# Optimization experiments

Measured on AMD Instinct MI355X. Metric: run time of the kernel, lower is better.

Reference implementation:

```python
import jax, jax.numpy as jnp
import numpy as np

B, F, HU, HC = 8192, 100, 128, 512


def _lin(key, din, dout, bias=True, scale=0.02):
    k1, k2 = jax.random.split(key)
    w = jax.random.normal(k1, (din, dout), jnp.float32) * scale
    if bias:
        b = jax.random.normal(k2, (dout,), jnp.float32) * scale
        return w, b
    return (w,)


def setup_inputs() -> dict:
    key = jax.random.key(0)
    ks = jax.random.split(key, 24)
    d = {}
    d['feature_list'] = jax.random.normal(ks[0], (B, F), jnp.float32)
    d['is_treat'] = jax.random.uniform(ks[1], (B,), jnp.float32)
    d['emb'] = jax.random.normal(ks[2], (F, HU), jnp.float32) * 0.02
    d['t_w'], d['t_b'] = _lin(ks[3], 1, HU)
    d['qw'], d['qb'] = _lin(ks[4], HU, HU)
    d['kw'], d['kb'] = _lin(ks[5], HU, HU)
    d['vw'], d['vb'] = _lin(ks[6], HU, HU)
    (d['a1w'],) = _lin(ks[7], HU, HU, bias=False)
    d['a2w'], d['a2b'] = _lin(ks[8], HU, HU)
    (d['a3w'],) = _lin(ks[9], HU, 1, bias=False)
    d['c1w'], d['c1b'] = _lin(ks[10], F * HU, HC)
    d['c2w'], d['c2b'] = _lin(ks[11], HC, HC)
    d['c3w'], d['c3b'] = _lin(ks[12], HC, HC // 2)
    d['c4w'], d['c4b'] = _lin(ks[13], HC // 2, HC // 4)
    d['c5w'], d['c5b'] = _lin(ks[14], HC // 4, HC // 8)
    d['clw'], d['clb'] = _lin(ks[15], HC // 8, 1)
    d['ctw'], d['ctb'] = _lin(ks[16], HC // 8, 1)
    d['u1w'], d['u1b'] = _lin(ks[17], HU, HU)
    d['u2w'], d['u2b'] = _lin(ks[18], HU, HU // 2)
    d['u3w'], d['u3b'] = _lin(ks[19], HU // 2, HU // 4)
    d['u4w'], d['u4b'] = _lin(ks[20], HU // 4, HU // 8)
    d['tlw'], d['tlb'] = _lin(ks[21], HU // 8, 1)
    d['utw'], d['utb'] = _lin(ks[22], HU // 8, 1)
    return d


def reference(feature_list, is_treat, emb, t_w, t_b, qw, qb, kw, kb, vw, vb,
              a1w, a2w, a2b, a3w, c1w, c1b, c2w, c2b, c3w, c3b, c4w, c4b,
              c5w, c5b, clw, clb, ctw, ctb, u1w, u1b, u2w, u2b, u3w, u3b,
              u4w, u4b, tlw, tlb, utw, utb):
    elu = jax.nn.elu
    sig = jax.nn.sigmoid
    b, f = feature_list.shape
    h = emb.shape[1]
    # per-feature embedding: [B, F, H]
    x_rep = feature_list[:, :, None] * emb[None, :, :]
    # normalize over the feature axis (dim=1), as in torch.linalg.norm(dim=1)
    nx = x_rep / jnp.linalg.norm(x_rep, axis=1, keepdims=True)
    # self-attention with sigmoid-then-softmax scores
    Q = nx @ qw + qb
    K = nx @ kw + kb
    V = nx @ vw + vb
    scores = jnp.einsum('bfh,bgh->bfg', Q, K) / (h ** 0.5)
    attn_w = jax.nn.softmax(sig(scores), axis=-1)
    xx = jnp.einsum('bfg,bgh->bfh', attn_w, V).reshape(b, f * h)
    # control net tower
    c = elu(xx @ c1w + c1b)
    c = elu(c @ c2w + c2b)
    c = elu(c @ c3w + c3b)
    c = elu(c @ c4w + c4b)
    c = elu(c @ c5w + c5b)  # is_self=True
    c_logit = c @ clw + clb
    c_tau = c @ ctw + ctb
    c_prob = sig(c_logit)
    # treatment representation: Linear(1, hu) on ones -> [B, H]
    t_rep = jnp.ones((b, 1), feature_list.dtype) @ t_w.reshape(1, h) + t_b
    # interaction attention (vectorized over features)
    att = jax.nn.relu(sig(t_rep @ a1w)[:, None, :] + sig(x_rep @ a2w + a2b))
    att = (att @ a3w)[..., 0]  # [B, F]
    attn = jax.nn.softmax(att, axis=1)
    xt = jnp.einsum('bf,bfh->bh', attn, x_rep)
    # uplift net tower
    u = elu(xt @ u1w + u1b)
    u = elu(u @ u2w + u2b)
    u = elu(u @ u3w + u3b)
    u = elu(u @ u4w + u4b)  # is_self=True
    t_logit = u @ tlw + tlb
    u_tau = u @ utw + utb
    t_prob = sig(t_logit)
    return (c_logit, c_prob, c_tau, t_logit, t_prob, u_tau)
```

## Files before the change

### kernel.cpp

```cpp
#include <hip/hip_runtime.h>
#include <hip/hip_bf16.h>

typedef __bf16 bf16;
typedef __bf16 bf16x8 __attribute__((ext_vector_type(8)));
typedef __bf16 bf16x4 __attribute__((ext_vector_type(4)));
typedef float f32x4 __attribute__((ext_vector_type(4)));
typedef unsigned u32x4 __attribute__((ext_vector_type(4)));

#define DEVI static __device__ __forceinline__

DEVI float sigmoidf_(float x){ return 1.0f/(1.0f+__expf(-x)); }
DEVI float eluf_(float x){ return x>0.f ? x : (__expf(x)-1.f); }
DEVI f32x4 mfma16(bf16x8 a, bf16x8 b, f32x4 c){ return __builtin_amdgcn_mfma_f32_16x16x32_bf16(a,b,c,0,0,0); }
DEVI f32x4 mfma8(long a, long b, f32x4 c){ return __builtin_amdgcn_mfma_f32_16x16x32_fp8_fp8(a,b,c,0,0,0); }
DEVI unsigned pack2_(float a, float b){
    union { bf16 v[2]; unsigned u; } t; t.v[0]=(bf16)a; t.v[1]=(bf16)b; return t.u;
}
DEVI unsigned long long pack4_(float a, float b, float c, float d){
    union { bf16 v[4]; unsigned long long u; } t;
    t.v[0]=(bf16)a; t.v[1]=(bf16)b; t.v[2]=(bf16)c; t.v[3]=(bf16)d; return t.u;
}
DEVI unsigned cvtfp8x4_(float a, float b, float c, float d){
    int v = __builtin_amdgcn_cvt_pk_fp8_f32(a, b, 0, false);
    v = __builtin_amdgcn_cvt_pk_fp8_f32(c, d, v, true);
    return (unsigned)v;
}
DEVI void gld16_(const void* g, void* l){
    __builtin_amdgcn_global_load_lds((const __attribute__((address_space(1))) void*)g,
                                     (__attribute__((address_space(3))) void*)l, 16, 0, 0);
}

#define B_ 8192
#define F_ 100
#define FP 112
#define H_ 128
#define KC_ 12800
#define SPLIT_ 4
#define FP8SC 16.0f

#define SWZ(r,bc) ((bc) ^ (((r)&7)<<4))
DEVI int swzk_(int row, int k){ return (k & ~127) | ((k & 127) ^ ((row&7)<<4)); }

DEVI void dotrans_(float (*t)[33], const float* in, bf16* out, int R, int C, int bx, int by, int tid){
    int c0 = bx*32, r0 = by*32;
    int tc = tid & 31, tr = tid >> 5;
    #pragma unroll
    for (int i=0;i<4;i++){
        int r = tr + i*8;
        t[r][tc] = in[(size_t)(r0+r)*C + c0 + tc];
    }
    __syncthreads();
    #pragma unroll
    for (int i=0;i<4;i++){
        int ro = tr + i*8;
        out[(size_t)(c0+ro)*R + r0 + tc] = (bf16)t[tc][ro];
    }
}

__global__ void k_prep_all(const float* __restrict__ qw, const float* __restrict__ qb,
                           const float* __restrict__ kw, const float* __restrict__ kb,
                           const float* __restrict__ tw, const float* __restrict__ tb,
                           const float* __restrict__ a1w, const float* __restrict__ vw,
                           const float* __restrict__ a2w, const float* __restrict__ c2w,
                           const float* __restrict__ c3w,
                           bf16* __restrict__ mextT, float* __restrict__ sigt, float* __restrict__ cconst,
                           bf16* __restrict__ wvT, bf16* __restrict__ wa2t,
                           bf16* __restrict__ c2wt, bf16* __restrict__ c3wt){
    __shared__ float t[32][33];
    const float rsc = 0.08838834764831845f;
    int blk = blockIdx.x, tid = threadIdx.x;
    if (blk < 9){
        #pragma unroll 1
        for (int e=0; e<8; ++e){
            int idx = e*256 + tid;
            int n = blk*16 + (idx>>7), h = idx&127;
            float acc = 0.f;
            if (n < 128){
                for (int d=0; d<128; ++d) acc += qw[h*128+d]*kw[n*128+d];
            } else if (n == 128){
                for (int d=0; d<128; ++d) acc += qw[h*128+d]*kb[d];
            } else if (n == 129){
                for (int d=0; d<128; ++d) acc += kw[h*128+d]*qb[d];
            }
            mextT[n*128+h] = (bf16)(acc*rsc);
        }
    } else if (blk == 9){
        if (tid < 128){
            float acc = 0.f;
            for (int h=0; h<128; ++h) acc += (tw[h]+tb[h]) * a1w[h*128+tid];
            sigt[tid] = sigmoidf_(acc);
        } else if (tid == 128){
            float acc = 0.f;
            for (int d=0; d<128; ++d) acc += qb[d]*kb[d];
            cconst[0] = acc*rsc;
        }
    } else if (blk < 26){
        int i = blk-10; dotrans_(t, vw, wvT, 128,128, i&3, i>>2, tid);
    } else if (blk < 42){
        int i = blk-26; dotrans_(t, a2w, wa2t, 128,128, i&3, i>>2, tid);
    } else if (blk < 298){
        int i = blk-42; dotrans_(t, c2w, c2wt, 512,512, i&15, i>>4, tid);
    } else {
        int i = blk-298; dotrans_(t, c3w, c3wt, 512,256, i&7, i>>3, tid);
    }
}

DEVI int kappa_(int k){
    int f = k>>7, h = k&127;
    if (f < 96)
        return (((f>>4)<<3) | (h>>4))*256 + ((f&15)>>2)*64 + (h&15)*4 + (f&3);
    else
        return 12288 + (h>>4)*64 + (h&15)*4 + (f&3);
}

__global__ __launch_bounds__(256,2) void k_gk(
    const float* __restrict__ c1w, unsigned char* __restrict__ c1wtk8,
    const float* __restrict__ feat, const float* __restrict__ emb,
    const bf16* __restrict__ wa2t, const float* __restrict__ a2b,
    const float* __restrict__ a3w, const float* __restrict__ sigt,
    float* __restrict__ attg)
{
    __shared__ char A[37888];
    int blk = blockIdx.x, tid = threadIdx.x;
    if (blk < 6400){
        float (*t)[33] = (float(*)[33])A;
        const int C = 512;
        int c0 = (blk&15)*32, r0 = (blk>>4)*32;
        int tc = tid & 31, tr = tid >> 5;
        #pragma unroll
        for (int i=0;i<4;i++){
            int r = tr + i*8;
            t[r][tc] = c1w[(size_t)(r0+r)*C + c0 + tc];
        }
        __syncthreads();
        #pragma unroll
        for (int i=0;i<4;i++){
            int ro = tr + i*8;
            float x = t[tc][ro]*FP8SC;
            int v = __builtin_amdgcn_cvt_pk_fp8_f32(x, x, 0, false);
            int n = c0+ro;
            c1wtk8[(size_t)n*KC_ + swzk_(n, kappa_(r0+tc))] = (unsigned char)v;
        }
        return;
    }
    bf16 (*sAt)[72] = (bf16(*)[72])A;
    bf16 (*sBt)[72] = (bf16(*)[72])(A + 18432);
    float (*sRed)[128] = (float(*)[128])(A + 36864);
    int w=tid>>6, lane=tid&63, l15=lane&15, l4=lane>>4;
    int m0 = (blk-6400)*128;
    int wr = w>>1, wc = w&1;
    f32x4 acc[4][4];
    #pragma unroll
    for(int mi=0;mi<4;mi++)
        #pragma unroll
        for(int ni=0;ni<4;ni++) acc[mi][ni] = (f32x4){0.f,0.f,0.f,0.f};

    #pragma unroll 1
    for (int k0=0; k0<128; k0+=64){
        __syncthreads();
        #pragma unroll
        for (int t4=0; t4<4; t4++){
            int t = tid + t4*256;
            int row=t>>3, col=(t&7)*8;
            int gr = m0+row;
            int bb = gr/112, ff = gr - bb*112;
            bf16x8 o;
            if (ff < F_){
                float fv = feat[(size_t)bb*F_ + ff];
                const float* ep = emb + ff*H_ + k0 + col;
                f32x4 e0 = *(const f32x4*)ep;
                f32x4 e1 = *(const f32x4*)(ep+4);
                o[0]=(bf16)(fv*e0[0]); o[1]=(bf16)(fv*e0[1]); o[2]=(bf16)(fv*e0[2]); o[3]=(bf16)(fv*e0[3]);
                o[4]=(bf16)(fv*e1[0]); o[5]=(bf16)(fv*e1[1]); o[6]=(bf16)(fv*e1[2]); o[7]=(bf16)(fv*e1[3]);
            } else {
                #pragma unroll
                for (int e=0;e<8;e++) o[e]=(bf16)0.f;
            }
            *(bf16x8*)&sAt[row][col] = o;
            *(bf16x8*)&sBt[row][col] = *(const bf16x8*)(wa2t + row*H_ + k0 + col);
        }
        __syncthreads();
        #pragma unroll
        for(int ks=0;ks<2;ks++){
            bf16x8 af[4], bfr[4];
            #pragma unroll
            for(int mi=0;mi<4;mi++) af[mi] = *(const bf16x8*)&sAt[wr*64+mi*16+l15][ks*32+l4*8];
            #pragma unroll
            for(int ni=0;ni<4;ni++) bfr[ni] = *(const bf16x8*)&sBt[wc*64+ni*16+l15][ks*32+l4*8];
            #pragma unroll
            for(int mi=0;mi<4;mi++)
                #pragma unroll
                for(int ni=0;ni<4;ni++)
                    acc[mi][ni] = mfma16(af[mi], bfr[ni], acc[mi][ni]);
        }
    }
    float sg[4], ab[4], a3[4];
    #pragma unroll
    for (int ni=0;ni<4;ni++){
        int n = wc*64 + ni*16 + l15;
        sg[ni]=sigt[n]; ab[ni]=a2b[n]; a3[ni]=a3w[n];
    }
    #pragma unroll
    for (int mi=0;mi<4;mi++){
        float sj[4] = {0.f,0.f,0.f,0.f};
        #pragma unroll
        for (int ni=0;ni<4;ni++){
            #pragma unroll
            for (int j=0;j<4;j++){
                float u = sigmoidf_(acc[mi][ni][j] + ab[ni]);
                float t = sg[ni] + u;
                t = t>0.f ? t : 0.f;
                sj[j] += t*a3[ni];
            }
        }
        #pragma unroll
        for (int j=0;j<4;j++){
            float v = sj[j];
            #pragma unroll
            for (int m=1;m<16;m<<=1) v += __shfl_xor(v,m,16);
            sj[j]=v;
        }
        if (l15==0){
            #pragma unroll
            for (int j=0;j<4;j++) sRed[wc][wr*64+mi*16+l4*4+j] = sj[j];
        }
    }
    __syncthreads();
    if (tid < 128) attg[(size_t)m0 + tid] = sRed[0][tid] + sRed[1][tid];
}

__global__ __launch_bounds__(512,2) void k_attn2(
    const float* __restrict__ feat, const float* __restrict__ emb,
    const bf16* __restrict__ mextT, const bf16* __restrict__ wvT,
    const float* __restrict__ vb, const float* __restrict__ cconst,
    const float* __restrict__ attg,
    unsigned char* __restrict__ xxb, bf16* __restrict__ xtb)
{
    __shared__ char L[81792];
    char* Lm = L;
    char* Ln = L + 32768;
    float* sFeat  = (float*)(L+61440);
    float* normP  = (float*)(L+62336);
    float* sAw    = (float*)(L+77568);
    float* sNorm  = (float*)(L+79872);
    float* sAlpha = (float*)(L+80384);
    float* sBeta  = (float*)(L+80832);
    float* sInv   = (float*)(L+81280);

    int b = blockIdx.x;
    int tid = threadIdx.x, w = tid>>6, lane = tid&63;
    int l15 = lane&15, l4 = lane>>4;
    bf16 (*sP)[72] = (bf16(*)[72])(L + 61440 + w*2304);

    bf16x8 awv[4];
    #pragma unroll
    for (int kc=0;kc<4;kc++)
        awv[kc] = *(const bf16x8*)(wvT + (w*16+l15)*H_ + kc*32 + l4*8);
    float vbr = vb[w*16+l15];

    #pragma unroll 2
    for (int v = tid; v < 128*16; v += 512){
        int n = v >> 4, cg = (v & 15) * 8;
        *(u32x4*)(Lm + n*256 + SWZ(n, cg*2)) = *(const u32x4*)(mextT + n*128 + cg);
    }
    if (tid < FP) sFeat[tid] = (tid<F_) ? feat[(size_t)b*F_+tid] : 0.f;
    if (w==0){
        const float* ag = attg + (size_t)b*FP;
        float a0 = (lane<F_)? ag[lane] : -1e30f;
        float a1 = (lane+64<F_)? ag[lane+64] : -1e30f;
        float m = fmaxf(a0,a1);
        #pragma unroll
        for(int s=1;s<64;s<<=1) m = fmaxf(m, __shfl_xor(m,s,64));
        float e0 = (lane<F_)? __expf(a0-m):0.f;
        float e1 = (lane+64<F_)? __expf(a1-m):0.f;
        float s = e0+e1;
        #pragma unroll
        for(int t=1;t<64;t<<=1) s += __shfl_xor(s,t,64);
        float inv = 1.f/s;
        if (lane<FP) sAw[lane] = e0*inv;
        if (lane+64<FP) sAw[lane+64] = e1*inv;
    }
    __syncthreads();

    int hp = (tid&63)*2, gg = tid>>6;
    {
        float fa0=0.f, fa1=0.f;
        #pragma unroll 4
        for (int it=0; it<13; ++it){
            int f = gg + 8*it;
            if (f < F_){
                float2 e2 = *(const float2*)(emb + f*H_ + hp);
                float v0 = sFeat[f]*e2.x, v1 = sFeat[f]*e2.y;
                fa0 += v0*v0; fa1 += v1*v1;
            }
        }
        *(float2*)(normP + gg*128 + hp) = make_float2(fa0, fa1);
    }
    __syncthreads();
    if (tid < 128){
        float s = 0.f;
        #pragma unroll
        for (int g2=0; g2<8; ++g2) s += normP[g2*128 + tid];
        sNorm[tid] = sqrtf(s);
    }
    __syncthreads();

    {
        float rn0 = __builtin_amdgcn_rcpf(sNorm[hp]);
        float rn1 = __builtin_amdgcn_rcpf(sNorm[hp+1]);
        #pragma unroll 4
        for (int it=0; it<13; ++it){
            int f = gg + 8*it;
            if (f < F_){
                float2 e2 = *(const float2*)(emb + f*H_ + hp);
                *(unsigned*)(Ln + f*256 + SWZ(f, hp*2)) = pack2_(sFeat[f]*e2.x*rn0, sFeat[f]*e2.y*rn1);
            }
        }
        for (int z=tid; z<768; z+=512){
            int f = 100 + (z>>6), hz = (z&63)*2;
            *(unsigned*)(Ln + f*256 + SWZ(f, hz*2)) = 0u;
        }
    }
    __syncthreads();

    int mt = w;

    if (mt < 7){
        bf16x8 bfr8[4];
        #pragma unroll
        for (int kc=0;kc<4;kc++)
            bfr8[kc] = *(const bf16x8*)(mextT + (128+(l15&1))*H_ + kc*32 + l4*8);
        f32x4 acc = {0.f,0.f,0.f,0.f};
        #pragma unroll
        for (int kc=0;kc<4;kc++){
            bf16x8 a = *(const bf16x8*)(Ln + (mt*16+l15)*256 + SWZ(mt*16+l15, (kc*32+l4*8)*2));
            acc = mfma16(a, bfr8[kc], acc);
        }
        if (l15==0){
            #pragma unroll
            for (int j=0;j<4;j++) sAlpha[mt*16+l4*4+j] = acc[j];
        }
        if (l15==1){
            #pragma unroll
            for (int j=0;j<4;j++) sBeta[mt*16+l4*4+j] = acc[j];
        }
    }
    __syncthreads();

    const float cc = cconst[0];
    unsigned long long uexB[3];
    if (mt < 7){
        bf16x8 afxi[4];
        #pragma unroll
        for (int kc=0;kc<4;kc++)
            afxi[kc] = *(const bf16x8*)(Ln + (mt*16+l15)*256 + SWZ(mt*16+l15, (kc*32+l4*8)*2));
        f32x4 sc[7];
        #pragma unroll
        for (int gt=0; gt<7; gt++) sc[gt] = (f32x4){0.f,0.f,0.f,0.f};
        #pragma unroll 1
        for (int p=0; p<2; p++){
            #pragma unroll 2
            for (int nt4=0; nt4<4; nt4++){
                int nt = p*4 + nt4;
                bf16x8 bw[4];
                #pragma unroll
                for (int kc=0;kc<4;kc++)
                    bw[kc] = *(const bf16x8*)(Lm + (nt*16+l15)*256 + SWZ(nt*16+l15, (kc*32+l4*8)*2));
                f32x4 d = {0.f,0.f,0.f,0.f};
                #pragma unroll
                for (int kc=0;kc<4;kc++) d = mfma16(bw[kc], afxi[kc], d);
                *(unsigned long long*)(&sP[l15][nt4*16 + l4*4]) = pack4_(d[0],d[1],d[2],d[3]);
            }
            bf16x8 afs0 = *(const bf16x8*)&sP[l15][l4*8];
            bf16x8 afs1 = *(const bf16x8*)&sP[l15][32+l4*8];
            #pragma unroll
            for (int gt=0; gt<7; gt++){
                int r = gt*16+l15;
                bf16x8 b0 = *(const bf16x8*)(Ln + r*256 + SWZ(r, (p*64 + l4*8)*2));
                bf16x8 b1 = *(const bf16x8*)(Ln + r*256 + SWZ(r, (p*64 + 32 + l4*8)*2));
                sc[gt] = mfma16(b0, afs0, sc[gt]);
                sc[gt] = mfma16(b1, afs1, sc[gt]);
            }
        }
        float aj = sAlpha[mt*16+l15];
        float rs = 0.f;
        #pragma unroll
        for (int gt=0; gt<7; gt++){
            f32x4 bt4 = *(const f32x4*)&sBeta[gt*16+l4*4];
            float e[4];
            #pragma unroll
            for (int j=0;j<4;j++){
                int g = gt*16 + l4*4 + j;
                float val = sc[gt][j] + aj + bt4[j] + cc;
                e[j] = (g<F_) ? __expf(sigmoidf_(val)) : 0.f;
                rs += e[j];
            }
            if (gt < 4)
                *(unsigned long long*)(&sP[l15][gt*16 + l4*4]) = pack4_(e[0],e[1],e[2],e[3]);
            else
                uexB[gt-4] = pack4_(e[0],e[1],e[2],e[3]);
        }
        rs += __shfl_xor(rs, 16, 64);
        rs += __shfl_xor(rs, 32, 64);
        if (l4 == 0) sInv[w*16 + l15] = 1.f/rs;
    } else {
        int h = lane;
        float a0=0.f, a1=0.f;
        #pragma unroll 4
        for (int f=0; f<F_; ++f){
            float awf = sAw[f];
            a0 += awf * (float)*(const bf16*)(Ln + f*256 + SWZ(f, h*2));
            a1 += awf * (float)*(const bf16*)(Ln + f*256 + SWZ(f, (h+64)*2));
        }
        xtb[(size_t)b*H_ + h]      = (bf16)(a0 * sNorm[h]);
        xtb[(size_t)b*H_ + h + 64] = (bf16)(a1 * sNorm[h+64]);
    }

    unsigned long long vpku[7];
    #pragma unroll
    for (int gt=0; gt<7; gt++){
        f32x4 acc = {0.f,0.f,0.f,0.f};
        #pragma unroll
        for (int kc=0;kc<4;kc++){
            int r = gt*16+l15;
            bf16x8 a = *(const bf16x8*)(Ln + r*256 + SWZ(r, (kc*32+l4*8)*2));
            acc = mfma16(a, awv[kc], acc);
        }
        vpku[gt] = pack4_(acc[0]+vbr, acc[1]+vbr, acc[2]+vbr, acc[3]+vbr);
    }
    __syncthreads();

    {
        int hrow = w*16 + l15;
        #pragma unroll
        for (int gt=0; gt<7; gt++)
            *(unsigned long long*)(Lm + hrow*256 + SWZ(hrow, gt*32 + l4*8)) = vpku[gt];
    }
    __syncthreads();

    if (mt < 7){
        bf16x8 ap0 = *(const bf16x8*)&sP[l15][l4*8];
        bf16x8 ap1 = *(const bf16x8*)&sP[l15][32+l4*8];
        f32x4 acc8[8];
        #pragma unroll
        for (int ht=0;ht<8;ht++) acc8[ht] = (f32x4){0.f,0.f,0.f,0.f};
        #pragma unroll
        for (int ht=0; ht<8; ht++){
            int r = ht*16+l15;
            bf16x8 bv0 = *(const bf16x8*)(Lm + r*256 + SWZ(r, (l4*8)*2));
            bf16x8 bv1 = *(const bf16x8*)(Lm + r*256 + SWZ(r, (32+l4*8)*2));
            acc8[ht] = mfma16(ap0, bv0, acc8[ht]);
            acc8[ht] = mfma16(ap1, bv1, acc8[ht]);
        }
        #pragma unroll
        for (int gt=4; gt<7; gt++)
            *(unsigned long long*)(&sP[l15][(gt-4)*16 + l4*4]) = uexB[gt-4];
        *(unsigned long long*)(&sP[l15][48 + l4*4]) = 0ull;
        bf16x8 ap2 = *(const bf16x8*)&sP[l15][l4*8];
        bf16x8 ap3 = *(const bf16x8*)&sP[l15][32+l4*8];
        #pragma unroll
        for (int ht=0; ht<8; ht++){
            int r = ht*16+l15;
            int c2 = 64+l4*8;
            int c3 = 96+l4*8;  if (c3 >= 112) c3 = 96;
            bf16x8 bv2 = *(const bf16x8*)(Lm + r*256 + SWZ(r, c2*2));
            bf16x8 bv3 = *(const bf16x8*)(Lm + r*256 + SWZ(r, c3*2));
            acc8[ht] = mfma16(ap2, bv2, acc8[ht]);
            acc8[ht] = mfma16(ap3, bv3, acc8[ht]);
        }
        float fs[4];
        #pragma unroll
        for (int j=0;j<4;j++) fs[j] = sInv[w*16 + l4*4 + j] * FP8SC;
        #pragma unroll
        for (int ht=0; ht<8; ht++){
            unsigned u = cvtfp8x4_(acc8[ht][0]*fs[0], acc8[ht][1]*fs[1], acc8[ht][2]*fs[2], acc8[ht][3]*fs[3]);
            if (mt < 6){
                *(unsigned*)(xxb + (size_t)b*KC_ + swzk_(b, (mt*8+ht)*256 + lane*4)) = u;
            } else if (l4 == 0){
                *(unsigned*)(xxb + (size_t)b*KC_ + swzk_(b, 12288 + ht*64 + l15*4)) = u;
            }
        }
    }
}

__global__ __launch_bounds__(512,2) void k_gemm_fp8(const unsigned char* __restrict__ A,
        const unsigned char* __restrict__ Bt, bf16* __restrict__ part, int M, int N, int K, int KS)
{
    __shared__ unsigned char S[49152];
    int tid=threadIdx.x, w=tid>>6, lane=tid&63, l15=lane&15, l4=lane>>4;
    int m0 = blockIdx.y*128, n0 = blockIdx.x*256;
    int kbeg = blockIdx.z*KS, kend = kbeg + KS;
    int wr = w>>2, wc = w&3;
    int offW = w*1024 + lane*16;
    int rS = offW >> 7, cS = offW & 127;
    f32x4 acc[4][4];
    #pragma unroll
    for(int mi=0;mi<4;mi++)
        #pragma unroll
        for(int ni=0;ni<4;ni++) acc[mi][ni] = (f32x4){0.f,0.f,0.f,0.f};

    int sx = (l15&7)<<4;

    for (int k0=kbeg; k0<kend; k0+=128){
        __syncthreads();
        gld16_(A + (size_t)(m0 + rS     )*K + k0 + cS, S + offW);
        gld16_(A + (size_t)(m0 + rS + 64)*K + k0 + cS, S + offW + 8192);
        #pragma unroll
        for (int q=0;q<4;q++)
            gld16_(Bt + (size_t)(n0 + q*64 + rS)*K + k0 + cS, S + 16384 + q*8192 + offW);
        __syncthreads();
        #pragma unroll
        for(int ks=0;ks<4;ks++){
            int co = (ks*32 + l4*8) ^ sx;
            long af[4], bfr[4];
            #pragma unroll
            for(int mi=0;mi<4;mi++) af[mi] = *(const long*)(S + (wr*64+mi*16+l15)*128 + co);
            #pragma unroll
            for(int ni=0;ni<4;ni++) bfr[ni] = *(const long*)(S + 16384 + (wc*64+ni*16+l15)*128 + co);
            #pragma unroll
            for(int mi=0;mi<4;mi++)
                #pragma unroll
                for(int ni=0;ni<4;ni++)
                    acc[mi][ni] = mfma8(af[mi], bfr[ni], acc[mi][ni]);
        }
    }
    bf16* pz = part + (size_t)blockIdx.z*M*N;
    #pragma unroll
    for(int mi=0;mi<4;mi++)
        #pragma unroll
        for(int ni=0;ni<4;ni++){
            int col = n0 + wc*64 + ni*16 + l15;
            #pragma unroll
            for(int j=0;j<4;j++){
                int row = m0 + wr*64 + mi*16 + l4*4 + j;
                pz[(size_t)row*N + col] = (bf16)acc[mi][ni][j];
            }
        }
}

__global__ void k_c1fin(const bf16* __restrict__ part, const float* __restrict__ bias,
                        bf16* __restrict__ out){
    const size_t MN = (size_t)B_*512;
    size_t e0 = ((size_t)blockIdx.x*256 + threadIdx.x)*4;
    bf16x4 p0 = *(const bf16x4*)(part + e0);
    bf16x4 p1 = *(const bf16x4*)(part + MN + e0);
    bf16x4 p2 = *(const bf16x4*)(part + 2*MN + e0);
    bf16x4 p3 = *(const bf16x4*)(part + 3*MN + e0);
    f32x4 bb = *(const f32x4*)(bias + (e0 & 511));
    const float ds = 1.0f/(FP8SC*FP8SC);
    float s0 = ((float)p0[0]+(float)p1[0]+(float)p2[0]+(float)p3[0])*ds + bb[0];
    float s1 = ((float)p0[1]+(float)p1[1]+(float)p2[1]+(float)p3[1])*ds + bb[1];
    float s2 = ((float)p0[2]+(float)p1[2]+(float)p2[2]+(float)p3[2])*ds + bb[2];
    float s3 = ((float)p0[3]+(float)p1[3]+(float)p2[3]+(float)p3[3])*ds + bb[3];
    unsigned long long u = pack4_(eluf_(s0), eluf_(s1), eluf_(s2), eluf_(s3));
    *(unsigned long long*)(out + e0) = u;
}

template<int BN, bool ELU>
__global__ __launch_bounds__(256,2) void k_gemm(const bf16* __restrict__ A, const bf16* __restrict__ Bt,
        const float* __restrict__ bias, bf16* __restrict__ out, int M, int N, int K)
{
    __shared__ bf16 sAt[128][72];
    __shared__ bf16 sBt[BN][72];
    int tid=threadIdx.x, w=tid>>6, lane=tid&63, l15=lane&15, l4=lane>>4;
    int m0 = blockIdx.y*128, n0 = blockIdx.x*BN;
    constexpr int MI = (BN==128)?4:2;
    constexpr int NI = (BN==128)?4:BN/16;
    int wr = (BN==128)? (w>>1) : w;
    int wc = (BN==128)? (w&1) : 0;
    f32x4 acc[MI][NI];
    #pragma unroll
    for(int mi=0;mi<MI;mi++)
        #pragma unroll
        for(int ni=0;ni<NI;ni++) acc[mi][ni] = (f32x4){0.f,0.f,0.f,0.f};

    for (int k0=0; k0<K; k0+=64){
        __syncthreads();
        for (int t=tid; t<128*8; t+=256){
            int row=t>>3, col=(t&7)*8;
            *(bf16x8*)&sAt[row][col] = *(const bf16x8*)(A + (size_t)(m0+row)*K + k0 + col);
        }
        for (int t=tid; t<BN*8; t+=256){
            int row=t>>3, col=(t&7)*8;
            *(bf16x8*)&sBt[row][col] = *(const bf16x8*)(Bt + (size_t)(n0+row)*K + k0 + col);
        }
        __syncthreads();
        #pragma unroll
        for(int ks=0;ks<2;ks++){
            bf16x8 af[MI], bfr[NI];
            #pragma unroll
            for(int mi=0;mi<MI;mi++) af[mi] = *(const bf16x8*)&sAt[wr*(MI*16)+mi*16+l15][ks*32+l4*8];
            #pragma unroll
            for(int ni=0;ni<NI;ni++) bfr[ni] = *(const bf16x8*)&sBt[wc*64+ni*16+l15][ks*32+l4*8];
            #pragma unroll
            for(int mi=0;mi<MI;mi++)
                #pragma unroll
                for(int ni=0;ni<NI;ni++)
                    acc[mi][ni] = mfma16(af[mi], bfr[ni], acc[mi][ni]);
        }
    }
    #pragma unroll
    for(int mi=0;mi<MI;mi++)
        #pragma unroll
        for(int ni=0;ni<NI;ni++){
            int col = n0 + wc*64 + ni*16 + l15;
            float bc = bias[col];
            #pragma unroll
            for(int j=0;j<4;j++){
                int row = m0 + wr*(MI*16) + mi*16 + l4*4 + j;
                float v = acc[mi][ni][j] + bc;
                if (ELU) v = eluf_(v);
                out[(size_t)row*N + col] = (bf16)v;
            }
        }
}

__global__ __launch_bounds__(256,2) void k_tails(const bf16* __restrict__ c3o,
    const float* __restrict__ c4w, const float* __restrict__ c4b,
    const float* __restrict__ c5w, const float* __restrict__ c5b,
    const float* __restrict__ clw, const float* __restrict__ clb,
    const float* __restrict__ ctw, const float* __restrict__ ctb,
    const bf16* __restrict__ xtb,
    const float* __restrict__ u1w, const float* __restrict__ u1b,
    const float* __restrict__ u2w, const float* __restrict__ u2b,
    const float* __restrict__ u3w, const float* __restrict__ u3b,
    const float* __restrict__ u4w, const float* __restrict__ u4b,
    const float* __restrict__ tlw, const float* __restrict__ tlb,
    const float* __restrict__ utw, const float* __restrict__ utb, float* __restrict__ outp)
{
    __shared__ char A[58880];
    int tid = threadIdx.x, blk = blockIdx.x;
    int r0 = (blk>>1)*32;
    if ((blk & 1) == 0){
        float (*sA)[260] = (float(*)[260])A;
        float (*sB)[132] = (float(*)[132])(A + 33280);
        float (*sC)[68]  = (float(*)[68])(A + 50176);
        for (int v=tid; v<32*64; v+=256){
            int r=v>>6, c=(v&63)*4;
            bf16x4 x = *(const bf16x4*)(c3o + (size_t)(r0+r)*256 + c);
            sA[r][c]=(float)x[0]; sA[r][c+1]=(float)x[1]; sA[r][c+2]=(float)x[2]; sA[r][c+3]=(float)x[3];
        }
        __syncthreads();
        {
            int j = tid&127, rb = tid>>7;
            float acc[16];
            #pragma unroll
            for (int i=0;i<16;i++) acc[i]=c4b[j];
            #pragma unroll 4
            for (int h=0;h<256;h++){
                float wv = c4w[h*128+j];
                #pragma unroll
                for (int i=0;i<16;i++) acc[i] += sA[2*i+rb][h]*wv;
            }
            #pragma unroll
            for (int i=0;i<16;i++) sB[2*i+rb][j] = eluf_(acc[i]);
        }
        __syncthreads();
        {
            int j = tid&63, rb = tid>>6;
            float acc[8];
            #pragma unroll
            for (int i=0;i<8;i++) acc[i]=c5b[j];
            #pragma unroll 4
            for (int h=0;h<128;h++){
                float wv = c5w[h*64+j];
                #pragma unroll
                for (int i=0;i<8;i++) acc[i] += sB[4*i+rb][h]*wv;
            }
            #pragma unroll
            for (int i=0;i<8;i++) sC[4*i+rb][j] = eluf_(acc[i]);
        }
        __syncthreads();
        if (tid < 32){
            float r1 = clb[0], r2 = ctb[0];
            #pragma unroll 8
            for (int k=0;k<64;k++){ float v = sC[tid][k]; r1 += v*clw[k]; r2 += v*ctw[k]; }
            int row = r0 + tid;
            outp[row] = r1;
            outp[B_ + row] = sigmoidf_(r1);
            outp[(size_t)2*B_ + row] = r2;
        }
    } else {
        float (*sA)[132] = (float(*)[132])A;
        float (*sB)[132] = (float(*)[132])(A + 16896);
        float (*sC)[68]  = (float(*)[68])(A + 33792);
        float (*sD)[36]  = (float(*)[36])(A + 42496);
        float (*sE)[20]  = (float(*)[20])(A + 47104);
        for (int v=tid; v<32*32; v+=256){
            int r=v>>5, c=(v&31)*4;
            bf16x4 x = *(const bf16x4*)(xtb + (size_t)(r0+r)*128 + c);
            sA[r][c]=(float)x[0]; sA[r][c+1]=(float)x[1]; sA[r][c+2]=(float)x[2]; sA[r][c+3]=(float)x[3];
        }
        __syncthreads();
        {
            int j = tid&127, rb = tid>>7;
            float acc[16];
            #pragma unroll
            for (int i=0;i<16;i++) acc[i]=u1b[j];
            #pragma unroll 4
            for (int h=0;h<128;h++){
                float wv = u1w[h*128+j];
                #pragma unroll
                for (int i=0;i<16;i++) acc[i] += sA[2*i+rb][h]*wv;
            }
            #pragma unroll
            for (int i=0;i<16;i++) sB[2*i+rb][j] = eluf_(acc[i]);
        }
        __syncthreads();
        {
            int j = tid&63, rb = tid>>6;
            float acc[8];
            #pragma unroll
            for (int i=0;i<8;i++) acc[i]=u2b[j];
            #pragma unroll 4
            for (int h=0;h<128;h++){
                float wv = u2w[h*64+j];
                #pragma unroll
                for (int i=0;i<8;i++) acc[i] += sB[4*i+rb][h]*wv;
            }
            #pragma unroll
            for (int i=0;i<8;i++) sC[4*i+rb][j] = eluf_(acc[i]);
        }
        __syncthreads();
        {
            int j = tid&31, rb = tid>>5;
            float acc[4];
            #pragma unroll
            for (int i=0;i<4;i++) acc[i]=u3b[j];
            #pragma unroll 4
            for (int h=0;h<64;h++){
                float wv = u3w[h*32+j];
                #pragma unroll
                for (int i=0;i<4;i++) acc[i] += sC[8*i+rb][h]*wv;
            }
            #pragma unroll
            for (int i=0;i<4;i++) sD[8*i+rb][j] = eluf_(acc[i]);
        }
        __syncthreads();
        {
            int j = tid&15, rb = tid>>4;
            float acc0=u4b[j], acc1=u4b[j];
            #pragma unroll 4
            for (int h=0;h<32;h++){
                float wv = u4w[h*16+j];
                acc0 += sD[rb][h]*wv;
                acc1 += sD[16+rb][h]*wv;
            }
            sE[rb][j] = eluf_(acc0);
            sE[16+rb][j] = eluf_(acc1);
        }
        __syncthreads();
        if (tid < 32){
            float r1 = tlb[0], r2 = utb[0];
            #pragma unroll
            for (int k=0;k<16;k++){ float v = sE[tid][k]; r1 += v*tlw[k]; r2 += v*utw[k]; }
            int row = r0 + tid;
            outp[(size_t)3*B_ + row] = r1;
            outp[(size_t)4*B_ + row] = sigmoidf_(r1);
            outp[(size_t)5*B_ + row] = r2;
        }
    }
}

extern "C" void kernel_launch(void* const* d_in, const int* in_sizes, int n_in,
                              void* d_out, int out_size, void* d_ws, size_t ws_size,
                              hipStream_t stream) {
    const float* feat=(const float*)d_in[0];
    const float* emb =(const float*)d_in[2];
    const float* t_w =(const float*)d_in[3]; const float* t_b=(const float*)d_in[4];
    const float* qw  =(const float*)d_in[5]; const float* qb =(const float*)d_in[6];
    const float* kw  =(const float*)d_in[7]; const float* kb =(const float*)d_in[8];
    const float* vw  =(const float*)d_in[9]; const float* vb =(const float*)d_in[10];
    const float* a1w =(const float*)d_in[11];
    const float* a2w =(const float*)d_in[12]; const float* a2b=(const float*)d_in[13];
    const float* a3w =(const float*)d_in[14];
    const float* c1w =(const float*)d_in[15]; const float* c1b=(const float*)d_in[16];
    const float* c2w =(const float*)d_in[17]; const float* c2b=(const float*)d_in[18];
    const float* c3w =(const float*)d_in[19]; const float* c3b=(const float*)d_in[20];
    const float* c4w =(const float*)d_in[21]; const float* c4b=(const float*)d_in[22];
    const float* c5w =(const float*)d_in[23]; const float* c5b=(const float*)d_in[24];
    const float* clw =(const float*)d_in[25]; const float* clb=(const float*)d_in[26];
    const float* ctw =(const float*)d_in[27]; const float* ctb=(const float*)d_in[28];
    const float* u1w =(const float*)d_in[29]; const float* u1b=(const float*)d_in[30];
    const float* u2w =(const float*)d_in[31]; const float* u2b=(const float*)d_in[32];
    const float* u3w =(const float*)d_in[33]; const float* u3b=(const float*)d_in[34];
    const float* u4w =(const float*)d_in[35]; const float* u4b=(const float*)d_in[36];
    const float* tlw =(const float*)d_in[37]; const float* tlb=(const float*)d_in[38];
    const float* utw =(const float*)d_in[39]; const float* utb=(const float*)d_in[40];
    float* outp = (float*)d_out;

    char* ws = (char*)d_ws;
    size_t off = 0;
    auto alloc = [&](size_t bytes)->char*{ char* p = ws + off; off += (bytes + 255) & ~(size_t)255; return p; };
    unsigned char* xxb = (unsigned char*)alloc((size_t)B_*KC_);
    bf16* part   = (bf16*)alloc((size_t)SPLIT_*B_*512*2);
    float* attg  = (float*)alloc((size_t)B_*FP*4);
    bf16* xtb    = (bf16*)alloc((size_t)B_*128*2);
    bf16* cbuf1  = (bf16*)alloc((size_t)B_*512*2);
    bf16* mextT  = (bf16*)alloc(144*128*2);
    bf16* wvT    = (bf16*)alloc(128*128*2);
    bf16* wa2t   = (bf16*)alloc(128*128*2);
    unsigned char* c1wtk8 = (unsigned char*)alloc((size_t)512*KC_);
    bf16* c2wt   = (bf16*)alloc((size_t)512*512*2);
    bf16* c3wt   = (bf16*)alloc((size_t)512*256*2);
    float* sigt  = (float*)alloc(128*4);
    float* cconst= (float*)alloc(4);
    bf16* cbuf2 = (bf16*)(xxb);
    bf16* cbuf3 = (bf16*)(xxb + (16u<<20));
    (void)ws_size; (void)in_sizes; (void)n_in; (void)out_size;

    k_prep_all<<<426,256,0,stream>>>(qw,qb,kw,kb,t_w,t_b,a1w, vw, a2w, c2w, c3w,
                                     mextT, sigt, cconst, wvT, wa2t, c2wt, c3wt);

    k_gk<<<13568,256,0,stream>>>(c1w, c1wtk8, feat, emb, wa2t, a2b, a3w, sigt, attg);

    k_attn2<<<B_,512,0,stream>>>(feat,emb,mextT,wvT,vb,cconst,attg, xxb, xtb);

    k_gemm_fp8<<<dim3(2,64,SPLIT_),512,0,stream>>>(xxb, c1wtk8, part, B_,512,KC_, KC_/SPLIT_);
    k_c1fin<<<4096,256,0,stream>>>(part, c1b, cbuf1);

    k_gemm<128,true><<<dim3(4,64),256,0,stream>>>(cbuf1, c2wt, c2b, cbuf2, B_,512,512);
    k_gemm<64,true><<<dim3(4,64),256,0,stream>>>(cbuf2, c3wt, c3b, cbuf3, B_,256,512);

    k_tails<<<512,256,0,stream>>>(cbuf3,c4w,c4b,c5w,c5b,clw,clb,ctw,ctb,
                                  xtb,u1w,u1b,u2w,u2b,u3w,u3b,u4w,u4b,tlw,tlb,utw,utb,outp);
}
```

Measured before the change: 620.8 us.

## Pre-swizzle c2/c3 GEMM operands and load tiles via direct global-to-LDS copies

The weight transposes, the c1 finalize and the c2 GEMM epilogue now write their outputs in an XOR-swizzled layout within each 128-byte chunk. The c2/c3 GEMMs use 16-byte direct global-to-LDS loads (gld16_) into unpadded tiles with a K step of 128, and read fragments with the matching swizzle. This is meant to cut the VGPR round trip and LDS bank conflicts on tile loads, and to halve the number of barrier-separated K iterations. In exchange, the producer and consumer layouts must agree exactly, and each block now uses more LDS.

```diff
diff --git a/kernel.cpp b/kernel.cpp
--- a/kernel.cpp
+++ b/kernel.cpp
@@ -54,6 +54,24 @@
     for (int i=0;i<4;i++){
         int ro = tr + i*8;
         out[(size_t)(c0+ro)*R + r0 + tc] = (bf16)t[tc][ro];
+    }
+}
+
+DEVI void dotrans_swz_(float (*t)[33], const float* in, bf16* out, int R, int C, int bx, int by, int tid){
+    int c0 = bx*32, r0 = by*32;
+    int tc = tid & 31, tr = tid >> 5;
+    #pragma unroll
+    for (int i=0;i<4;i++){
+        int r = tr + i*8;
+        t[r][tc] = in[(size_t)(r0+r)*C + c0 + tc];
+    }
+    __syncthreads();
+    #pragma unroll
+    for (int i=0;i<4;i++){
+        int ro = tr + i*8;
+        int n = c0+ro;
+        int ob = swzk_(n, (r0+tc)*2);
+        *(bf16*)((char*)out + (size_t)n*R*2 + ob) = (bf16)t[tc][ro];
     }
 }
 
@@ -99,9 +117,9 @@
     } else if (blk < 42){
         int i = blk-26; dotrans_(t, a2w, wa2t, 128,128, i&3, i>>2, tid);
     } else if (blk < 298){
-        int i = blk-42; dotrans_(t, c2w, c2wt, 512,512, i&15, i>>4, tid);
+        int i = blk-42; dotrans_swz_(t, c2w, c2wt, 512,512, i&15, i>>4, tid);
     } else {
-        int i = blk-298; dotrans_(t, c3w, c3wt, 512,256, i&7, i>>3, tid);
+        int i = blk-298; dotrans_swz_(t, c3w, c3wt, 512,256, i&7, i>>3, tid);
     }
 }
 
@@ -553,64 +571,72 @@
     float s2 = ((float)p0[2]+(float)p1[2]+(float)p2[2]+(float)p3[2])*ds + bb[2];
     float s3 = ((float)p0[3]+(float)p1[3]+(float)p2[3]+(float)p3[3])*ds + bb[3];
     unsigned long long u = pack4_(eluf_(s0), eluf_(s1), eluf_(s2), eluf_(s3));
-    *(unsigned long long*)(out + e0) = u;
-}
-
-template<int BN, bool ELU>
-__global__ __launch_bounds__(256,2) void k_gemm(const bf16* __restrict__ A, const bf16* __restrict__ Bt,
+    int row = (int)(e0 >> 9);
+    int ob = swzk_(row, (int)(e0 & 511) * 2);
+    *(unsigned long long*)((char*)out + (size_t)row*1024 + ob) = u;
+}
+
+template<int BN, bool SWZOUT>
+__global__ __launch_bounds__(256,2) void k_gemm_g(const bf16* __restrict__ A, const bf16* __restrict__ Bt,
         const float* __restrict__ bias, bf16* __restrict__ out, int M, int N, int K)
 {
-    __shared__ bf16 sAt[128][72];
-    __shared__ bf16 sBt[BN][72];
+    __shared__ unsigned char S[32768 + BN*256];
     int tid=threadIdx.x, w=tid>>6, lane=tid&63, l15=lane&15, l4=lane>>4;
     int m0 = blockIdx.y*128, n0 = blockIdx.x*BN;
     constexpr int MI = (BN==128)?4:2;
-    constexpr int NI = (BN==128)?4:BN/16;
     int wr = (BN==128)? (w>>1) : w;
     int wc = (BN==128)? (w&1) : 0;
-    f32x4 acc[MI][NI];
+    int offT = tid*16;
+    int rS = offT >> 8, cS = offT & 255;
+    f32x4 acc[MI][4];
     #pragma unroll
     for(int mi=0;mi<MI;mi++)
         #pragma unroll
-        for(int ni=0;ni<NI;ni++) acc[mi][ni] = (f32x4){0.f,0.f,0.f,0.f};
-
-    for (int k0=0; k0<K; k0+=64){
-        __syncthreads();
-        for (int t=tid; t<128*8; t+=256){
-            int row=t>>3, col=(t&7)*8;
-            *(bf16x8*)&sAt[row][col] = *(const bf16x8*)(A + (size_t)(m0+row)*K + k0 + col);
-        }
-        for (int t=tid; t<BN*8; t+=256){
-            int row=t>>3, col=(t&7)*8;
-            *(bf16x8*)&sBt[row][col] = *(const bf16x8*)(Bt + (size_t)(n0+row)*K + k0 + col);
-        }
-        __syncthreads();
-        #pragma unroll
-        for(int ks=0;ks<2;ks++){
-            bf16x8 af[MI], bfr[NI];
-            #pragma unroll
-            for(int mi=0;mi<MI;mi++) af[mi] = *(const bf16x8*)&sAt[wr*(MI*16)+mi*16+l15][ks*32+l4*8];
-            #pragma unroll
-            for(int ni=0;ni<NI;ni++) bfr[ni] = *(const bf16x8*)&sBt[wc*64+ni*16+l15][ks*32+l4*8];
+        for(int ni=0;ni<4;ni++) acc[mi][ni] = (f32x4){0.f,0.f,0.f,0.f};
+
+    int sx = (l15&7)<<4;
+
+    for (int k0=0; k0<K; k0+=128){
+        __syncthreads();
+        #pragma unroll
+        for (int q=0;q<8;q++)
+            gld16_((const char*)A + ((size_t)(m0 + q*16 + rS)*K + k0)*2 + cS, S + q*4096 + offT);
+        #pragma unroll
+        for (int q=0;q<BN/16;q++)
+            gld16_((const char*)Bt + ((size_t)(n0 + q*16 + rS)*K + k0)*2 + cS, S + 32768 + q*4096 + offT);
+        __syncthreads();
+        #pragma unroll
+        for(int ks=0;ks<4;ks++){
+            int co = (ks*32 + l4*8)*2;
+            co = (co & ~127) | ((co & 127) ^ sx);
+            bf16x8 af[MI], bfr[4];
+            #pragma unroll
+            for(int mi=0;mi<MI;mi++) af[mi] = *(const bf16x8*)(S + (wr*(MI*16)+mi*16+l15)*256 + co);
+            #pragma unroll
+            for(int ni=0;ni<4;ni++) bfr[ni] = *(const bf16x8*)(S + 32768 + (wc*64+ni*16+l15)*256 + co);
             #pragma unroll
             for(int mi=0;mi<MI;mi++)
                 #pragma unroll
-                for(int ni=0;ni<NI;ni++)
+                for(int ni=0;ni<4;ni++)
                     acc[mi][ni] = mfma16(af[mi], bfr[ni], acc[mi][ni]);
         }
     }
     #pragma unroll
     for(int mi=0;mi<MI;mi++)
         #pragma unroll
-        for(int ni=0;ni<NI;ni++){
+        for(int ni=0;ni<4;ni++){
             int col = n0 + wc*64 + ni*16 + l15;
             float bc = bias[col];
             #pragma unroll
             for(int j=0;j<4;j++){
                 int row = m0 + wr*(MI*16) + mi*16 + l4*4 + j;
-                float v = acc[mi][ni][j] + bc;
-                if (ELU) v = eluf_(v);
-                out[(size_t)row*N + col] = (bf16)v;
+                float v = eluf_(acc[mi][ni][j] + bc);
+                if (SWZOUT){
+                    int ob = swzk_(row, col*2);
+                    *(bf16*)((char*)out + (size_t)row*N*2 + ob) = (bf16)v;
+                } else {
+                    out[(size_t)row*N + col] = (bf16)v;
+                }
             }
         }
 }
@@ -819,8 +845,8 @@
     k_gemm_fp8<<<dim3(2,64,SPLIT_),512,0,stream>>>(xxb, c1wtk8, part, B_,512,KC_, KC_/SPLIT_);
     k_c1fin<<<4096,256,0,stream>>>(part, c1b, cbuf1);
 
-    k_gemm<128,true><<<dim3(4,64),256,0,stream>>>(cbuf1, c2wt, c2b, cbuf2, B_,512,512);
-    k_gemm<64,true><<<dim3(4,64),256,0,stream>>>(cbuf2, c3wt, c3b, cbuf3, B_,256,512);
+    k_gemm_g<128,true><<<dim3(4,64),256,0,stream>>>(cbuf1, c2wt, c2b, cbuf2, B_,512,512);
+    k_gemm_g<64,false><<<dim3(4,64),256,0,stream>>>(cbuf2, c3wt, c3b, cbuf3, B_,256,512);
 
     k_tails<<<512,256,0,stream>>>(cbuf3,c4w,c4b,c5w,c5b,clw,clb,ctw,ctb,
                                   xtb,u1w,u1b,u2w,u2b,u3w,u3b,u4w,u4b,tlw,tlb,utw,utb,outp);
```

Measured after the change: 597.4 us (median of 2 runs). 1.04x faster.
